# Optimization experiments

Hardware: AMD Instinct MI355X
Metric: run time of the kernel (lower is better)

The kernel has to match this reference:

```python
import jax, jax.numpy as jnp
import numpy as np

B = 256; NROIS = 200; IN = 200; HID = 128; L = 4; H = 8; RATIO = 0.5
K = int(np.ceil(RATIO * NROIS))        # SAGPooling top-k per graph = 100
N = B * NROIS                          # total nodes = 51200
DEG = 32; EPG = NROIS * DEG; E_EDGES = B * EPG  # 1,638,400 edges
EMB = HID * L                          # MHA embed dim = 512
DH = EMB // H

def _xavier(k, shape):
    fan_in, fan_out = shape[-2], shape[-1]
    lim = float(np.sqrt(6.0 / (fan_in + fan_out)))
    return jax.random.uniform(k, shape, jnp.float32, -lim, lim)

def setup_inputs() -> dict:
    key = jax.random.key(0)
    ks = jax.random.split(key, 16)
    x = jax.random.normal(ks[0], (N, IN), jnp.float32)
    # block-diagonal edge list: edges stay within each graph's node range
    src = jax.random.randint(ks[1], (E_EDGES,), 0, NROIS, jnp.int32)
    dst = jax.random.randint(ks[2], (E_EDGES,), 0, NROIS, jnp.int32)
    off = jnp.repeat(jnp.arange(B, dtype=jnp.int32) * NROIS, EPG)
    edge_index = jnp.stack([src + off, dst + off])
    edge_attr = jax.random.normal(ks[3], (E_EDGES,), jnp.float32)  # unused by the math
    batch = jnp.repeat(jnp.arange(B, dtype=jnp.int32), NROIS)
    return dict(
        x=x, edge_index=edge_index, edge_attr=edge_attr, batch=batch,
        gcn_w0=_xavier(ks[4], (IN, HID)),
        gcn_w=_xavier(ks[5], (L - 1, HID, HID)),
        gcn_b=jnp.zeros((L, HID), jnp.float32),
        lin1_w0=_xavier(ks[6], (IN + HID, HID)),
        lin1_w=_xavier(ks[7], (L - 1, 2 * HID, HID)),
        lin1_b=jnp.zeros((L, HID), jnp.float32),
        lin2_w=_xavier(ks[8], (L, HID, HID)),
        lin2_b=jnp.zeros((L, HID), jnp.float32),
        sag_w1=_xavier(ks[9], (HID, 1)),
        sag_w2=_xavier(ks[10], (HID, 1)),
        sag_b=jnp.zeros((1,), jnp.float32),
        mha_in_w=_xavier(ks[11], (3 * EMB, EMB)),
        mha_in_b=jnp.zeros((3 * EMB,), jnp.float32),
        mha_out_w=_xavier(ks[12], (EMB, EMB)),
        mha_out_b=jnp.zeros((EMB,), jnp.float32),
        fin_w=_xavier(ks[13], (EMB, HID)),
        fin_b=jnp.zeros((HID,), jnp.float32),
    )

def _gcn_conv(x, src, dst, W, b):
    xw = x @ W
    deg = jax.ops.segment_sum(jnp.ones_like(dst, jnp.float32), dst, num_segments=N) + 1.0
    dinv = jax.lax.rsqrt(deg)
    norm = dinv[src] * dinv[dst]                     # [E]
    agg = jax.ops.segment_sum(xw[src] * norm[:, None], dst, num_segments=N)
    agg = agg + xw * (dinv * dinv)[:, None]          # self-loop term
    return agg + b

def _gcblock(x, src, dst, gw, gb, l1w, l1b, l2w, l2b):
    x1 = jnp.tanh(_gcn_conv(x, src, dst, gw, gb))
    h = jnp.tanh(jnp.concatenate([x, x1], axis=1) @ l1w + l1b)
    return jnp.tanh(h @ l2w + l2b)

def _sag_pool_pad(z, src, dst, w1, w2, b):
    # SAGPooling score via PyG GraphConv (aggr='add'): lin_rel(sum_j x_j) + lin_root(x_i)
    neigh = jax.ops.segment_sum(z[src], dst, num_segments=N)
    score = (neigh @ w1)[:, 0] + b[0] + (z @ w2)[:, 0]        # [N]
    s3 = score.reshape(B, NROIS)
    vals, idx = jax.lax.top_k(s3, K)                           # [B,K]
    z3 = z.reshape(B, NROIS, HID)
    pooled = jnp.take_along_axis(z3, idx[:, :, None], axis=1) * jnp.tanh(vals)[:, :, None]
    zpad = jnp.zeros_like(z3).at[jnp.arange(B)[:, None], idx].set(pooled)
    return zpad.reshape(N, HID)

def reference(x, edge_index, edge_attr, batch,
              gcn_w0, gcn_w, gcn_b, lin1_w0, lin1_w, lin1_b, lin2_w, lin2_b,
              sag_w1, sag_w2, sag_b,
              mha_in_w, mha_in_b, mha_out_w, mha_out_b, fin_w, fin_b):
    src, dst = edge_index[0], edge_index[1]
    z = x
    pads = []
    for i in range(L):
        gw = gcn_w0 if i == 0 else gcn_w[i - 1]
        l1w = lin1_w0 if i == 0 else lin1_w[i - 1]
        z = _gcblock(z, src, dst, gw, gcn_b[i], l1w, lin1_b[i], lin2_w[i], lin2_b[i])
        pads.append(_sag_pool_pad(z, src, dst, sag_w1, sag_w2, sag_b))
    xc = jnp.concatenate(pads, axis=1).reshape(B, NROIS, EMB)   # [B,S,E]
    # MultiheadAttention (batch_first, eval mode -> no dropout)
    qkv = xc @ mha_in_w.T + mha_in_b                             # [B,S,3E]
    q, k, v = jnp.split(qkv, 3, axis=-1)
    def heads(t):
        return t.reshape(B, NROIS, H, DH).transpose(0, 2, 1, 3)  # [B,H,S,dh]
    q, k, v = heads(q), heads(k), heads(v)
    scores = jnp.einsum('bhqd,bhkd->bhqk', q, k) / np.sqrt(DH)
    attn = jax.nn.softmax(scores, axis=-1)                       # [B,H,S,S]
    o = jnp.einsum('bhqk,bhkd->bhqd', attn, v).transpose(0, 2, 1, 3).reshape(B, NROIS, EMB)
    o = o @ mha_out_w.T + mha_out_b
    attn_weights = attn.mean(axis=1)                             # avg over heads [B,S,S]
    # readout: global_mean_pool over each graph's nrois nodes
    pooled = o.mean(axis=1)                                      # [B,E]
    out = jnp.tanh(pooled @ fin_w + fin_b)                       # [B,HID]
    return out, attn_weights
```

## Files before the change

kernel.cpp:

```cpp
#include <hip/hip_runtime.h>
#include <hip/hip_fp16.h>


#define GB   256
#define SS   200
#define KIN  200
#define HD   128
#define NLAY 4
#define NHD  8
#define TOPK 100
#define NT   (GB * SS)
#define EPG_ 6400
#define NE_  (GB * EPG_)
#define EMB_ 512

typedef _Float16 half8 __attribute__((ext_vector_type(8)));
typedef _Float16 half4v __attribute__((ext_vector_type(4)));
typedef float floatx4 __attribute__((ext_vector_type(4)));

__global__ __launch_bounds__(256) void k_build_A(const int* __restrict__ src,
                                                 const int* __restrict__ dst,
                                                 float* __restrict__ A) {
  int e = blockIdx.x * 256 + threadIdx.x;
  if (e >= NE_) return;
  int d = dst[e], s = src[e];
  int b = d / SS;
  int dl = d - b * SS;
  int sl = s - b * SS;
  atomicAdd(&A[((size_t)b * SS + dl) * SS + sl], 1.0f);
}

__global__ __launch_bounds__(256) void k_dinv(const float* __restrict__ A,
                                              float* __restrict__ dinv) {
  int node = blockIdx.x * 4 + (threadIdx.x >> 6);
  int lane = threadIdx.x & 63;
  const float* r = A + (size_t)node * SS;
  float v = r[lane] + r[lane + 64] + r[lane + 128];
  if (lane < 8) v += r[lane + 192];
#pragma unroll
  for (int o = 32; o; o >>= 1) v += __shfl_xor(v, o);
  if (lane == 0) dinv[node] = rsqrtf(v + 1.0f);
}

__global__ __launch_bounds__(256) void k_prep_all(
    const float* __restrict__ gcn_w0, const float* __restrict__ gcn_w,
    const float* __restrict__ lin1_w0, const float* __restrict__ lin1_w,
    const float* __restrict__ lin2_w,
    __half* __restrict__ whi, __half* __restrict__ wlo) {
  const int mat = blockIdx.x >> 7;
  const int n   = blockIdx.x & 127;
  const int l = mat / 3, which = mat % 3;
  const float* src;
  int K, Kpad;
  if (which == 0) {
    K = l ? HD : KIN;  Kpad = l ? 128 : 256;
    src = l ? gcn_w + (size_t)(l - 1) * HD * HD : gcn_w0;
  } else if (which == 1) {
    K = l ? 2 * HD : KIN + HD;  Kpad = l ? 256 : 384;
    src = l ? lin1_w + (size_t)(l - 1) * 2 * HD * HD : lin1_w0;
  } else {
    K = HD;  Kpad = HD;
    src = lin2_w + (size_t)l * HD * HD;
  }
  int off = (l == 0) ? (which == 0 ? 0 : (which == 1 ? 32768 : 81920))
                     : 98304 + (l - 1) * 65536 +
                       (which == 0 ? 0 : (which == 1 ? 16384 : 49152));
  _Float16* wh = (_Float16*)whi + (size_t)off + (size_t)n * Kpad;
  _Float16* wl = (_Float16*)wlo + (size_t)off + (size_t)n * Kpad;
  for (int k = threadIdx.x; k < Kpad; k += 256) {
    float v = (k < K) ? src[(size_t)k * HD + n] : 0.f;
    _Float16 h = (_Float16)v;
    wh[k] = h;
    wl[k] = (_Float16)(v - (float)h);
  }
}

__global__ __launch_bounds__(256) void k_node_mfma(
    const float* __restrict__ in1, int k1,
    const float* __restrict__ in2,
    const __half* __restrict__ Whi, const __half* __restrict__ Wlo,
    int Kpad,
    const float* __restrict__ bias,
    float* __restrict__ out, int doTanh) {
  const int m0 = blockIdx.x * 64;
  const int t = threadIdx.x;
  const int wave = t >> 6, lane = t & 63;
  const int col = lane & 15, quad = lane >> 4;
  const int wm = (wave & 1) * 32;
  const int wn = (wave >> 1) * 64;
  __shared__ __align__(16) _Float16 Ah[64][72];
  __shared__ __align__(16) _Float16 Al[64][72];
  floatx4 acc[2][4] = {};
  const int lr = t >> 2;
  const int lk = (t & 3) * 16;
  const _Float16* Wh = (const _Float16*)Whi;
  const _Float16* Wl = (const _Float16*)Wlo;

  for (int k0 = 0; k0 < Kpad; k0 += 64) {
    __syncthreads();
#pragma unroll
    for (int q = 0; q < 4; ++q) {
      int kg = k0 + lk + q * 4;
      float4 v = {0.f, 0.f, 0.f, 0.f};
      if (kg < k1)
        v = *reinterpret_cast<const float4*>(&in1[(size_t)(m0 + lr) * k1 + kg]);
      else if (in2 && kg < k1 + HD)
        v = *reinterpret_cast<const float4*>(&in2[(size_t)(m0 + lr) * HD + (kg - k1)]);
      half4v h = {(_Float16)v.x, (_Float16)v.y, (_Float16)v.z, (_Float16)v.w};
      half4v lo = {(_Float16)(v.x - (float)h.x), (_Float16)(v.y - (float)h.y),
                   (_Float16)(v.z - (float)h.z), (_Float16)(v.w - (float)h.w)};
      *reinterpret_cast<half4v*>(&Ah[lr][lk + q * 4]) = h;
      *reinterpret_cast<half4v*>(&Al[lr][lk + q * 4]) = lo;
    }
    __syncthreads();
#pragma unroll
    for (int ks = 0; ks < 2; ++ks) {
      half8 ah[2], al[2], bh[4], bl[4];
#pragma unroll
      for (int i = 0; i < 2; ++i) {
        ah[i] = *reinterpret_cast<const half8*>(&Ah[wm + i * 16 + col][ks * 32 + quad * 8]);
        al[i] = *reinterpret_cast<const half8*>(&Al[wm + i * 16 + col][ks * 32 + quad * 8]);
      }
#pragma unroll
      for (int j = 0; j < 4; ++j) {
        const size_t wo = (size_t)(wn + j * 16 + col) * Kpad + k0 + ks * 32 + quad * 8;
        bh[j] = *reinterpret_cast<const half8*>(Wh + wo);
        bl[j] = *reinterpret_cast<const half8*>(Wl + wo);
      }
#pragma unroll
      for (int i = 0; i < 2; ++i)
#pragma unroll
        for (int j = 0; j < 4; ++j) {
          acc[i][j] = __builtin_amdgcn_mfma_f32_16x16x32_f16(ah[i], bh[j], acc[i][j], 0, 0, 0);
          acc[i][j] = __builtin_amdgcn_mfma_f32_16x16x32_f16(ah[i], bl[j], acc[i][j], 0, 0, 0);
          acc[i][j] = __builtin_amdgcn_mfma_f32_16x16x32_f16(al[i], bh[j], acc[i][j], 0, 0, 0);
        }
    }
  }
#pragma unroll
  for (int j = 0; j < 4; ++j) {
    int n = wn + j * 16 + col;
    float bb = bias ? bias[n] : 0.f;
#pragma unroll
    for (int i = 0; i < 2; ++i) {
      int rbase = m0 + wm + i * 16 + quad * 4;
#pragma unroll
      for (int r = 0; r < 4; ++r) {
        float v = acc[i][j][r] + bb;
        if (doTanh) v = tanhf(v);
        out[(size_t)(rbase + r) * HD + n] = v;
      }
    }
  }
}

__global__ __launch_bounds__(256) void k_agg_mfma(
    const float* __restrict__ A, const float* __restrict__ dinv,
    const float* __restrict__ xw, const float* __restrict__ bias,
    float* __restrict__ out) {
  const int b    = blockIdx.x >> 1;
  const int row0 = (blockIdx.x & 1) * 128;
  const int t = threadIdx.x;
  const int wave = t >> 6, lane = t & 63;
  const int col = lane & 15, quad = lane >> 4;
  const int wm = (wave & 1) * 64, wn = (wave >> 1) * 64;
  __shared__ __align__(16) _Float16 Ah[128][72];
  __shared__ __align__(16) _Float16 Al[128][72];
  __shared__ __align__(16) _Float16 Bh[128][72];
  __shared__ __align__(16) _Float16 Bl[128][72];
  __shared__ float dvs[256];
  dvs[t] = (t < SS) ? dinv[b * SS + t] : 0.f;
  floatx4 acc[4][4] = {};
  const float* Ab  = A  + (size_t)b * SS * SS;
  const float* xwb = xw + (size_t)b * SS * HD;
  const int lr = t >> 1, lk = (t & 1) * 32;
  const int d = row0 + lr;
  __syncthreads();
  const float dvd = (d < SS) ? dvs[d] : 0.f;

  for (int k0 = 0; k0 < 256; k0 += 64) {
    __syncthreads();
#pragma unroll
    for (int q = 0; q < 8; ++q) {
      int s = k0 + lk + q * 4;
      float4 v = {0.f, 0.f, 0.f, 0.f};
      if (d < SS && s < SS)
        v = *reinterpret_cast<const float4*>(&Ab[(size_t)d * SS + s]);
      float e0 = (v.x + ((s + 0 == d) ? 1.f : 0.f)) * dvd * dvs[(s + 0) & 255];
      float e1 = (v.y + ((s + 1 == d) ? 1.f : 0.f)) * dvd * dvs[(s + 1) & 255];
      float e2 = (v.z + ((s + 2 == d) ? 1.f : 0.f)) * dvd * dvs[(s + 2) & 255];
      float e3 = (v.w + ((s + 3 == d) ? 1.f : 0.f)) * dvd * dvs[(s + 3) & 255];
      half4v h = {(_Float16)e0, (_Float16)e1, (_Float16)e2, (_Float16)e3};
      half4v lo = {(_Float16)(e0 - (float)h.x), (_Float16)(e1 - (float)h.y),
                   (_Float16)(e2 - (float)h.z), (_Float16)(e3 - (float)h.w)};
      *reinterpret_cast<half4v*>(&Ah[lr][lk + q * 4]) = h;
      *reinterpret_cast<half4v*>(&Al[lr][lk + q * 4]) = lo;
    }
#pragma unroll
    for (int p = 0; p < 8; ++p) {
      int idx = t + p * 256;
      int c4 = idx & 31, ss = idx >> 5;
      int s = k0 + ss;
      float4 v = {0.f, 0.f, 0.f, 0.f};
      if (s < SS)
        v = *reinterpret_cast<const float4*>(&xwb[(size_t)s * HD + c4 * 4]);
      int ssx = ss ^ ((c4 & 7) << 3);
      float e[4] = {v.x, v.y, v.z, v.w};
#pragma unroll
      for (int j = 0; j < 4; ++j) {
        _Float16 h = (_Float16)e[j];
        Bh[c4 * 4 + j][ssx] = h;
        Bl[c4 * 4 + j][ssx] = (_Float16)(e[j] - (float)h);
      }
    }
    __syncthreads();
#pragma unroll
    for (int ks = 0; ks < 2; ++ks) {
      half8 ah[4], al[4], bh[4], bl[4];
#pragma unroll
      for (int i = 0; i < 4; ++i) {
        ah[i] = *reinterpret_cast<const half8*>(&Ah[wm + i * 16 + col][ks * 32 + quad * 8]);
        al[i] = *reinterpret_cast<const half8*>(&Al[wm + i * 16 + col][ks * 32 + quad * 8]);
      }
#pragma unroll
      for (int j = 0; j < 4; ++j) {
        int n = wn + j * 16 + col;
        int koff = (ks * 32 + quad * 8) ^ (((n >> 2) & 7) << 3);
        bh[j] = *reinterpret_cast<const half8*>(&Bh[n][koff]);
        bl[j] = *reinterpret_cast<const half8*>(&Bl[n][koff]);
      }
#pragma unroll
      for (int i = 0; i < 4; ++i)
#pragma unroll
        for (int j = 0; j < 4; ++j) {
          acc[i][j] = __builtin_amdgcn_mfma_f32_16x16x32_f16(ah[i], bh[j], acc[i][j], 0, 0, 0);
          acc[i][j] = __builtin_amdgcn_mfma_f32_16x16x32_f16(ah[i], bl[j], acc[i][j], 0, 0, 0);
          acc[i][j] = __builtin_amdgcn_mfma_f32_16x16x32_f16(al[i], bh[j], acc[i][j], 0, 0, 0);
        }
    }
  }
#pragma unroll
  for (int j = 0; j < 4; ++j) {
    int n = wn + j * 16 + col;
    float bb = bias[n];
#pragma unroll
    for (int i = 0; i < 4; ++i) {
      int rbase = row0 + wm + i * 16 + quad * 4;
#pragma unroll
      for (int r = 0; r < 4; ++r) {
        int row = rbase + r;
        if (row < SS)
          out[((size_t)b * SS + row) * HD + n] = tanhf(acc[i][j][r] + bb);
      }
    }
  }
}

__global__ __launch_bounds__(256) void k_sag(
    const float* __restrict__ z, const float* __restrict__ A,
    const float* __restrict__ w1, const float* __restrict__ w2,
    const float* __restrict__ sb, float* __restrict__ xc, int layer) {
  const int b = blockIdx.x, t = threadIdx.x;
  __shared__ float w1s[HD], w2s[HD];
  __shared__ float zw1[SS], sc[SS], fac[SS];
  if (t < HD) { w1s[t] = w1[t]; w2s[t] = w2[t]; }
  __syncthreads();
  float a2 = 0.f;
  if (t < SS) {
    const float4* zr = reinterpret_cast<const float4*>(&z[((size_t)b * SS + t) * HD]);
    float a1 = 0.f;
#pragma unroll
    for (int q = 0; q < HD / 4; ++q) {
      float4 v = zr[q];
      a1 += v.x * w1s[4 * q] + v.y * w1s[4 * q + 1] + v.z * w1s[4 * q + 2] + v.w * w1s[4 * q + 3];
      a2 += v.x * w2s[4 * q] + v.y * w2s[4 * q + 1] + v.z * w2s[4 * q + 2] + v.w * w2s[4 * q + 3];
    }
    zw1[t] = a1;
  }
  __syncthreads();
  if (t < SS) {
    float s = sb[0] + a2;
    const float4* ar = reinterpret_cast<const float4*>(&A[((size_t)b * SS + t) * SS]);
#pragma unroll 5
    for (int q = 0; q < SS / 4; ++q) {
      float4 v = ar[q];
      s += v.x * zw1[4 * q] + v.y * zw1[4 * q + 1] + v.z * zw1[4 * q + 2] + v.w * zw1[4 * q + 3];
    }
    sc[t] = s;
  }
  __syncthreads();
  if (t < SS) {
    float si = sc[t];
    int cnt = 0;
    for (int j = 0; j < SS; ++j) {
      float sj = sc[j];
      cnt += (sj > si || (sj == si && j < t)) ? 1 : 0;
    }
    fac[t] = (cnt < TOPK) ? tanhf(si) : 0.f;
  }
  __syncthreads();
  for (int idx = t; idx < SS * HD; idx += 256) {
    int row = idx >> 7, c = idx & 127;
    xc[((size_t)b * SS + row) * EMB_ + layer * HD + c] =
        fac[row] * z[((size_t)b * SS + row) * HD + c];
  }
}

__global__ __launch_bounds__(256) void k_proj(
    const float* __restrict__ xc, const float* __restrict__ Win,
    const float* __restrict__ bin, __half* __restrict__ QKh) {
  const int wg = (blockIdx.x & 7) * 400 + (blockIdx.x >> 3);
  const int bm = wg >> 3;
  const int bn = wg & 7;
  const int m0 = bm * 128, n0 = bn * 128;
  const int t    = threadIdx.x;
  const int wave = t >> 6, lane = t & 63;
  const int col  = lane & 15, quad = lane >> 4;
  const int wm = (wave & 1) * 64;
  const int wn = (wave >> 1) * 64;
  __shared__ __align__(16) _Float16 As[128][72];
  __shared__ __align__(16) _Float16 Bs[128][72];
  floatx4 acc[4][4] = {};
  const int lr = t >> 1;
  const int lk = (t & 1) * 32;

  for (int k0 = 0; k0 < EMB_; k0 += 64) {
    __syncthreads();
    const float4* ga = reinterpret_cast<const float4*>(&xc [(size_t)(m0 + lr) * EMB_ + k0 + lk]);
    const float4* gb = reinterpret_cast<const float4*>(&Win[(size_t)(n0 + lr) * EMB_ + k0 + lk]);
#pragma unroll
    for (int q = 0; q < 8; ++q) {
      float4 va = ga[q];
      half4v ha = {(_Float16)va.x, (_Float16)va.y, (_Float16)va.z, (_Float16)va.w};
      *reinterpret_cast<half4v*>(&As[lr][lk + q * 4]) = ha;
      float4 vb = gb[q];
      half4v hb = {(_Float16)vb.x, (_Float16)vb.y, (_Float16)vb.z, (_Float16)vb.w};
      *reinterpret_cast<half4v*>(&Bs[lr][lk + q * 4]) = hb;
    }
    __syncthreads();
#pragma unroll
    for (int ks = 0; ks < 2; ++ks) {
      half8 af[4], bf[4];
#pragma unroll
      for (int i = 0; i < 4; ++i)
        af[i] = *reinterpret_cast<const half8*>(&As[wm + i * 16 + col][ks * 32 + quad * 8]);
#pragma unroll
      for (int j = 0; j < 4; ++j)
        bf[j] = *reinterpret_cast<const half8*>(&Bs[wn + j * 16 + col][ks * 32 + quad * 8]);
#pragma unroll
      for (int i = 0; i < 4; ++i)
#pragma unroll
        for (int j = 0; j < 4; ++j)
          acc[i][j] = __builtin_amdgcn_mfma_f32_16x16x32_f16(af[i], bf[j], acc[i][j], 0, 0, 0);
    }
  }
#pragma unroll
  for (int j = 0; j < 4; ++j) {
    int c = n0 + wn + j * 16 + col;
    float bb = bin[c];
#pragma unroll
    for (int i = 0; i < 4; ++i) {
      int rbase = m0 + wm + i * 16 + quad * 4;
#pragma unroll
      for (int r = 0; r < 4; ++r)
        QKh[(size_t)(rbase + r) * 1024 + c] = __float2half(acc[i][j][r] + bb);
    }
  }
}

__global__ __launch_bounds__(256) void k_attn(
    const __half* __restrict__ QKh,
    float* __restrict__ cpbuf,
    float* __restrict__ attn) {
  const int b  = blockIdx.x / 13;
  const int it = blockIdx.x % 13;
  const int i0 = it * 16;
  const int rows = (SS - i0 >= 16) ? 16 : (SS - i0);
  const int t    = threadIdx.x;
  const int wave = t >> 6;
  const int lane = t & 63;
  const int col  = lane & 15;
  const int quad = lane >> 4;

  __shared__ __align__(16) _Float16 kS[208][72];
  __shared__ __align__(16) _Float16 qS[16][72];
  __shared__ __align__(16) float    Ss[16][212];

  float am[13];
  int   soff[13];
  int   kmax = 0;
#pragma unroll
  for (int k = 0; k < 13; ++k) {
    int idx = t + (k << 8);
    am[k] = 0.f;
    if (idx < rows * 200) {
      int i = idx / 200;
      soff[k] = idx + 12 * i;
      kmax = k + 1;
    } else soff[k] = 0;
  }

  const size_t gbase = (size_t)b * SS * 1024;

  for (int h = 0; h < NHD; ++h) {
    __syncthreads();
#pragma unroll
    for (int p = 0; p < 7; ++p) {
      int li = t + (p << 8);
      if (li < 1664) {
        int j = li >> 3, c = li & 7;
        float4 v = {0.f, 0.f, 0.f, 0.f};
        if (j < SS) v = *reinterpret_cast<const float4*>(
            &QKh[gbase + (size_t)j * 1024 + 512 + h * 64 + c * 8]);
        *reinterpret_cast<float4*>(&kS[j][c * 8]) = v;
      }
    }
    if (t < 128) {
      int i = t >> 3, c = t & 7;
      int gi = i0 + i;
      float4 v = {0.f, 0.f, 0.f, 0.f};
      if (gi < SS) v = *reinterpret_cast<const float4*>(
          &QKh[gbase + (size_t)gi * 1024 + h * 64 + c * 8]);
      *reinterpret_cast<float4*>(&qS[i][c * 8]) = v;
    }
    __syncthreads();
    half8 a0 = *reinterpret_cast<const half8*>(&qS[col][quad * 8]);
    half8 a1 = *reinterpret_cast<const half8*>(&qS[col][32 + quad * 8]);
#pragma unroll
    for (int m = 0; m < 4; ++m) {
      int jt = wave + m * 4;
      if (jt < 13) {
        const int j0 = jt * 16;
        half8 b0 = *reinterpret_cast<const half8*>(&kS[j0 + col][quad * 8]);
        half8 b1 = *reinterpret_cast<const half8*>(&kS[j0 + col][32 + quad * 8]);
        floatx4 acc = {0.f, 0.f, 0.f, 0.f};
        acc = __builtin_amdgcn_mfma_f32_16x16x32_f16(a0, b0, acc, 0, 0, 0);
        acc = __builtin_amdgcn_mfma_f32_16x16x32_f16(a1, b1, acc, 0, 0, 0);
#pragma unroll
        for (int r = 0; r < 4; ++r)
          Ss[quad * 4 + r][j0 + col] = acc[r] * 0.125f;
      }
    }
    __syncthreads();
#pragma unroll
    for (int ri = 0; ri < 4; ++ri) {
      int r = wave * 4 + ri;
      if (r < rows) {
        float* srow = &Ss[r][0];
        float s0 = srow[lane], s1 = srow[lane + 64], s2 = srow[lane + 128];
        float s3 = (lane < 8) ? srow[lane + 192] : -1e30f;
        float mx = fmaxf(fmaxf(s0, s1), fmaxf(s2, s3));
#pragma unroll
        for (int o = 32; o; o >>= 1) mx = fmaxf(mx, __shfl_xor(mx, o));
        float e0 = __expf(s0 - mx), e1 = __expf(s1 - mx), e2 = __expf(s2 - mx);
        float e3 = (lane < 8) ? __expf(s3 - mx) : 0.f;
        float sum = e0 + e1 + e2 + e3;
#pragma unroll
        for (int o = 32; o; o >>= 1) sum += __shfl_xor(sum, o);
        float rl = 1.0f / sum;
        srow[lane] = e0 * rl; srow[lane + 64] = e1 * rl; srow[lane + 128] = e2 * rl;
        if (lane < 8) srow[lane + 192] = e3 * rl;
      }
    }
    __syncthreads();
    const float* sflat = &Ss[0][0];
#pragma unroll
    for (int k = 0; k < 13; ++k)
      if (k < kmax) am[k] += sflat[soff[k]] * 0.125f;
    if (t < SS) {
      float s = 0.f;
      for (int i = 0; i < rows; ++i) s += Ss[i][t];
      atomicAdd(&cpbuf[((size_t)b * NHD + h) * SS + t], s);
    }
  }
  float* abase = &attn[((size_t)b * SS + i0) * SS];
#pragma unroll
  for (int k = 0; k < 13; ++k)
    if (k < kmax) abase[t + (k << 8)] = am[k];
}

__global__ __launch_bounds__(256) void k_pool(
    const float* __restrict__ xc, const float* __restrict__ cpbuf,
    const float* __restrict__ Win, const float* __restrict__ bin,
    float* __restrict__ pooled) {
  const int b = blockIdx.x, t = threadIdx.x;
  __shared__ float cps[NHD][SS];
  __shared__ float tvs[NHD][EMB_];
  for (int idx = t; idx < NHD * SS; idx += 256) {
    int h = idx / SS, j = idx - h * SS;
    cps[h][j] = cpbuf[((size_t)b * NHD + h) * SS + j];
  }
  __syncthreads();
  const float* xcb = xc + (size_t)b * SS * EMB_;
  float a0[NHD] = {0.f}, a1[NHD] = {0.f};
  for (int j = 0; j < SS; ++j) {
    float x0 = xcb[(size_t)j * EMB_ + t];
    float x1 = xcb[(size_t)j * EMB_ + t + 256];
#pragma unroll
    for (int h = 0; h < NHD; ++h) {
      float c = cps[h][j];
      a0[h] += c * x0; a1[h] += c * x1;
    }
  }
#pragma unroll
  for (int h = 0; h < NHD; ++h) { tvs[h][t] = a0[h]; tvs[h][t + 256] = a1[h]; }
  __syncthreads();
  const int wv = t >> 6, lane = t & 63;
  for (int e = wv; e < EMB_; e += 4) {
    int h = e >> 6;
    const float* wr = Win + (size_t)(2 * EMB_ + e) * EMB_;
    float s = 0.f;
#pragma unroll
    for (int q = 0; q < 8; ++q) s += wr[lane + q * 64] * tvs[h][lane + q * 64];
#pragma unroll
    for (int o = 32; o; o >>= 1) s += __shfl_xor(s, o);
    if (lane == 0) pooled[(size_t)b * EMB_ + e] = bin[2 * EMB_ + e] * (float)SS + s;
  }
}

__global__ __launch_bounds__(256) void k_final(
    const float* __restrict__ pooled, const float* __restrict__ Wout,
    const float* __restrict__ bout, const float* __restrict__ finw,
    const float* __restrict__ finb, float* __restrict__ out) {
  const int b = blockIdx.x, t = threadIdx.x;
  __shared__ float pl[EMB_], po[EMB_];
  for (int k = t; k < EMB_; k += 256) pl[k] = pooled[(size_t)b * EMB_ + k] * (1.0f / (float)SS);
  __syncthreads();
  for (int e = t; e < EMB_; e += 256) {
    const float* wr = &Wout[(size_t)e * EMB_];
    float a = bout[e];
    for (int k = 0; k < EMB_; ++k) a += wr[k] * pl[k];
    po[e] = a;
  }
  __syncthreads();
  if (t < HD) {
    float a = finb[t];
    for (int e = 0; e < EMB_; ++e) a += po[e] * finw[(size_t)e * HD + t];
    out[(size_t)b * HD + t] = tanhf(a);
  }
}

extern "C" void kernel_launch(void* const* d_in, const int* in_sizes, int n_in,
                              void* d_out, int out_size, void* d_ws, size_t ws_size,
                              hipStream_t stream) {
  const float* x         = (const float*)d_in[0];
  const int*   ei        = (const int*)d_in[1];
  const float* gcn_w0    = (const float*)d_in[4];
  const float* gcn_w     = (const float*)d_in[5];
  const float* gcn_b     = (const float*)d_in[6];
  const float* lin1_w0   = (const float*)d_in[7];
  const float* lin1_w    = (const float*)d_in[8];
  const float* lin1_b    = (const float*)d_in[9];
  const float* lin2_w    = (const float*)d_in[10];
  const float* lin2_b    = (const float*)d_in[11];
  const float* sag_w1    = (const float*)d_in[12];
  const float* sag_w2    = (const float*)d_in[13];
  const float* sag_b     = (const float*)d_in[14];
  const float* mha_in_w  = (const float*)d_in[15];
  const float* mha_in_b  = (const float*)d_in[16];
  const float* mha_out_w = (const float*)d_in[17];
  const float* mha_out_b = (const float*)d_in[18];
  const float* fin_w     = (const float*)d_in[19];
  const float* fin_b     = (const float*)d_in[20];

  float* ws     = (float*)d_ws;
  float* dinv   = ws;
  float* Araw   = dinv + NT;
  float* buf0   = Araw + (size_t)GB * SS * SS;
  float* buf1   = buf0 + (size_t)NT * HD;
  float* zbuf   = buf1 + (size_t)NT * HD;
  float* xcbuf  = zbuf + (size_t)NT * HD;
  float* pooled = xcbuf + (size_t)NT * EMB_;
  __half* QKh  = (__half*)Araw;
  float* cpbuf = Araw + 26214400;

  float* outp = (float*)d_out;
  float* attn = outp + (size_t)GB * HD;

  __half* whi = (__half*)attn;
  __half* wlo = whi + 294912;

  hipMemsetAsync(Araw, 0, (size_t)GB * SS * SS * sizeof(float), stream);

  k_prep_all<<<12 * 128, 256, 0, stream>>>(gcn_w0, gcn_w, lin1_w0, lin1_w, lin2_w, whi, wlo);
  k_build_A<<<NE_ / 256, 256, 0, stream>>>(ei, ei + NE_, Araw);
  k_dinv<<<NT / 4, 256, 0, stream>>>(Araw, dinv);

  static const int KPg[4]  = {256, 128, 128, 128};
  static const int KP1[4]  = {384, 256, 256, 256};
  static const int OFFg[4] = {0, 98304, 163840, 229376};
  static const int OFF1[4] = {32768, 114688, 180224, 245760};
  static const int OFF2[4] = {81920, 147456, 212992, 278528};

  for (int l = 0; l < NLAY; ++l) {
    const float* zin = (l == 0) ? x : zbuf;
    int k1 = (l == 0) ? KIN : HD;
    k_node_mfma<<<NT / 64, 256, 0, stream>>>(zin, k1, nullptr,
                                             whi + OFFg[l], wlo + OFFg[l], KPg[l],
                                             nullptr, buf0, 0);
    k_agg_mfma<<<GB * 2, 256, 0, stream>>>(Araw, dinv, buf0, gcn_b + l * HD, buf1);
    k_node_mfma<<<NT / 64, 256, 0, stream>>>(zin, k1, buf1,
                                             whi + OFF1[l], wlo + OFF1[l], KP1[l],
                                             lin1_b + l * HD, buf0, 1);
    k_node_mfma<<<NT / 64, 256, 0, stream>>>(buf0, HD, nullptr,
                                             whi + OFF2[l], wlo + OFF2[l], HD,
                                             lin2_b + l * HD, zbuf, 1);
    k_sag<<<GB, 256, 0, stream>>>(zbuf, Araw, sag_w1, sag_w2, sag_b, xcbuf, l);
  }

  hipMemsetAsync(cpbuf, 0, (size_t)GB * NHD * SS * sizeof(float), stream);
  k_proj<<<(NT / 128) * 8, 256, 0, stream>>>(xcbuf, mha_in_w, mha_in_b, QKh);
  k_attn<<<GB * 13, 256, 0, stream>>>(QKh, cpbuf, attn);
  k_pool<<<GB, 256, 0, stream>>>(xcbuf, cpbuf, mha_in_w, mha_in_b, pooled);
  k_final<<<GB, 256, 0, stream>>>(pooled, mha_out_w, mha_out_b, fin_w, fin_b, outp);
}
```

Baseline: 1.624 ms.

## Store xc as fp16 hi/lo pairs and read QK/MHA operands directly from global

k_sag now writes the concatenated pooled features as fp16 high/low pairs instead of fp32. A new prep kernel converts the MHA input weights to fp16 once. k_proj then feeds its MFMA fragments straight from global memory with no LDS staging or in-loop conversion, and k_attn likewise reads Q/K fragments from global, with its block order swizzled for cache locality. k_pool rebuilds fp32 values from the hi/lo pair. The aim is to cut conversion work, shared-memory traffic and barriers, at the cost of uncoalesced-looking global fragment loads that rely on L2 hits.

```diff
diff --git a/kernel.cpp b/kernel.cpp
--- a/kernel.cpp
+++ b/kernel.cpp
@@ -73,6 +73,14 @@
     wh[k] = h;
     wl[k] = (_Float16)(v - (float)h);
   }
+}
+
+__global__ __launch_bounds__(256) void k_prep_w16(const float* __restrict__ W,
+                                                  __half* __restrict__ W16) {
+  int i = blockIdx.x * 256 + threadIdx.x;
+  float4 v = reinterpret_cast<const float4*>(W)[i];
+  half4v h = {(_Float16)v.x, (_Float16)v.y, (_Float16)v.z, (_Float16)v.w};
+  *reinterpret_cast<half4v*>((_Float16*)W16 + (size_t)i * 4) = h;
 }
 
 __global__ __launch_bounds__(256) void k_node_mfma(
@@ -259,7 +267,8 @@
 __global__ __launch_bounds__(256) void k_sag(
     const float* __restrict__ z, const float* __restrict__ A,
     const float* __restrict__ w1, const float* __restrict__ w2,
-    const float* __restrict__ sb, float* __restrict__ xc, int layer) {
+    const float* __restrict__ sb,
+    __half* __restrict__ xch, __half* __restrict__ xcl, int layer) {
   const int b = blockIdx.x, t = threadIdx.x;
   __shared__ float w1s[HD], w2s[HD];
   __shared__ float zw1[SS], sc[SS], fac[SS];
@@ -299,60 +308,54 @@
     fac[t] = (cnt < TOPK) ? tanhf(si) : 0.f;
   }
   __syncthreads();
+  _Float16* xh = (_Float16*)xch;
+  _Float16* xl = (_Float16*)xcl;
   for (int idx = t; idx < SS * HD; idx += 256) {
     int row = idx >> 7, c = idx & 127;
-    xc[((size_t)b * SS + row) * EMB_ + layer * HD + c] =
-        fac[row] * z[((size_t)b * SS + row) * HD + c];
+    float v = fac[row] * z[((size_t)b * SS + row) * HD + c];
+    _Float16 h = (_Float16)v;
+    size_t o = ((size_t)b * SS + row) * EMB_ + layer * HD + c;
+    xh[o] = h;
+    xl[o] = (_Float16)(v - (float)h);
   }
 }
 
 __global__ __launch_bounds__(256) void k_proj(
-    const float* __restrict__ xc, const float* __restrict__ Win,
+    const __half* __restrict__ xch, const __half* __restrict__ Win16,
     const float* __restrict__ bin, __half* __restrict__ QKh) {
   const int wg = (blockIdx.x & 7) * 400 + (blockIdx.x >> 3);
   const int bm = wg >> 3;
   const int bn = wg & 7;
   const int m0 = bm * 128, n0 = bn * 128;
-  const int t    = threadIdx.x;
+  const int t = threadIdx.x;
   const int wave = t >> 6, lane = t & 63;
-  const int col  = lane & 15, quad = lane >> 4;
+  const int col = lane & 15, quad = lane >> 4;
   const int wm = (wave & 1) * 64;
   const int wn = (wave >> 1) * 64;
-  __shared__ __align__(16) _Float16 As[128][72];
-  __shared__ __align__(16) _Float16 Bs[128][72];
   floatx4 acc[4][4] = {};
-  const int lr = t >> 1;
-  const int lk = (t & 1) * 32;
-
-  for (int k0 = 0; k0 < EMB_; k0 += 64) {
-    __syncthreads();
-    const float4* ga = reinterpret_cast<const float4*>(&xc [(size_t)(m0 + lr) * EMB_ + k0 + lk]);
-    const float4* gb = reinterpret_cast<const float4*>(&Win[(size_t)(n0 + lr) * EMB_ + k0 + lk]);
-#pragma unroll
-    for (int q = 0; q < 8; ++q) {
-      float4 va = ga[q];
-      half4v ha = {(_Float16)va.x, (_Float16)va.y, (_Float16)va.z, (_Float16)va.w};
-      *reinterpret_cast<half4v*>(&As[lr][lk + q * 4]) = ha;
-      float4 vb = gb[q];
-      half4v hb = {(_Float16)vb.x, (_Float16)vb.y, (_Float16)vb.z, (_Float16)vb.w};
-      *reinterpret_cast<half4v*>(&Bs[lr][lk + q * 4]) = hb;
-    }
-    __syncthreads();
-#pragma unroll
-    for (int ks = 0; ks < 2; ++ks) {
-      half8 af[4], bf[4];
-#pragma unroll
-      for (int i = 0; i < 4; ++i)
-        af[i] = *reinterpret_cast<const half8*>(&As[wm + i * 16 + col][ks * 32 + quad * 8]);
+  const _Float16* X = (const _Float16*)xch;
+  const _Float16* W = (const _Float16*)Win16;
+  const _Float16* xa[4];
+  const _Float16* wb[4];
+#pragma unroll
+  for (int i = 0; i < 4; ++i)
+    xa[i] = X + (size_t)(m0 + wm + i * 16 + col) * EMB_ + quad * 8;
+#pragma unroll
+  for (int j = 0; j < 4; ++j)
+    wb[j] = W + (size_t)(n0 + wn + j * 16 + col) * EMB_ + quad * 8;
+
+#pragma unroll 4
+  for (int k0 = 0; k0 < EMB_; k0 += 32) {
+    half8 af[4], bf[4];
+#pragma unroll
+    for (int i = 0; i < 4; ++i) af[i] = *reinterpret_cast<const half8*>(xa[i] + k0);
+#pragma unroll
+    for (int j = 0; j < 4; ++j) bf[j] = *reinterpret_cast<const half8*>(wb[j] + k0);
+#pragma unroll
+    for (int i = 0; i < 4; ++i)
 #pragma unroll
       for (int j = 0; j < 4; ++j)
-        bf[j] = *reinterpret_cast<const half8*>(&Bs[wn + j * 16 + col][ks * 32 + quad * 8]);
-#pragma unroll
-      for (int i = 0; i < 4; ++i)
-#pragma unroll
-        for (int j = 0; j < 4; ++j)
-          acc[i][j] = __builtin_amdgcn_mfma_f32_16x16x32_f16(af[i], bf[j], acc[i][j], 0, 0, 0);
-    }
+        acc[i][j] = __builtin_amdgcn_mfma_f32_16x16x32_f16(af[i], bf[j], acc[i][j], 0, 0, 0);
   }
 #pragma unroll
   for (int j = 0; j < 4; ++j) {
@@ -372,8 +375,9 @@
     const __half* __restrict__ QKh,
     float* __restrict__ cpbuf,
     float* __restrict__ attn) {
-  const int b  = blockIdx.x / 13;
-  const int it = blockIdx.x % 13;
+  const int bx = (blockIdx.x & 7) * 416 + (blockIdx.x >> 3);
+  const int b  = bx / 13;
+  const int it = bx % 13;
   const int i0 = it * 16;
   const int rows = (SS - i0 >= 16) ? 16 : (SS - i0);
   const int t    = threadIdx.x;
@@ -382,9 +386,7 @@
   const int col  = lane & 15;
   const int quad = lane >> 4;
 
-  __shared__ __align__(16) _Float16 kS[208][72];
-  __shared__ __align__(16) _Float16 qS[16][72];
-  __shared__ __align__(16) float    Ss[16][212];
+  __shared__ __align__(16) float Ss[16][212];
 
   float am[13];
   int   soff[13];
@@ -400,45 +402,31 @@
     } else soff[k] = 0;
   }
 
-  const size_t gbase = (size_t)b * SS * 1024;
+  const _Float16* Qbase = (const _Float16*)QKh + (size_t)b * SS * 1024;
+  const _Float16* qrow = Qbase + (size_t)(i0 + col) * 1024 + quad * 8;
+  const _Float16* krow[4];
+#pragma unroll
+  for (int m = 0; m < 4; ++m) {
+    int jt = wave + m * 4;
+    krow[m] = Qbase + (size_t)(jt * 16 + col) * 1024 + 512 + quad * 8;
+  }
 
   for (int h = 0; h < NHD; ++h) {
-    __syncthreads();
-#pragma unroll
-    for (int p = 0; p < 7; ++p) {
-      int li = t + (p << 8);
-      if (li < 1664) {
-        int j = li >> 3, c = li & 7;
-        float4 v = {0.f, 0.f, 0.f, 0.f};
-        if (j < SS) v = *reinterpret_cast<const float4*>(
-            &QKh[gbase + (size_t)j * 1024 + 512 + h * 64 + c * 8]);
-        *reinterpret_cast<float4*>(&kS[j][c * 8]) = v;
-      }
-    }
-    if (t < 128) {
-      int i = t >> 3, c = t & 7;
-      int gi = i0 + i;
-      float4 v = {0.f, 0.f, 0.f, 0.f};
-      if (gi < SS) v = *reinterpret_cast<const float4*>(
-          &QKh[gbase + (size_t)gi * 1024 + h * 64 + c * 8]);
-      *reinterpret_cast<float4*>(&qS[i][c * 8]) = v;
-    }
-    __syncthreads();
-    half8 a0 = *reinterpret_cast<const half8*>(&qS[col][quad * 8]);
-    half8 a1 = *reinterpret_cast<const half8*>(&qS[col][32 + quad * 8]);
+    const int hoff = h * 64;
+    half8 a0 = *reinterpret_cast<const half8*>(qrow + hoff);
+    half8 a1 = *reinterpret_cast<const half8*>(qrow + hoff + 32);
 #pragma unroll
     for (int m = 0; m < 4; ++m) {
       int jt = wave + m * 4;
       if (jt < 13) {
-        const int j0 = jt * 16;
-        half8 b0 = *reinterpret_cast<const half8*>(&kS[j0 + col][quad * 8]);
-        half8 b1 = *reinterpret_cast<const half8*>(&kS[j0 + col][32 + quad * 8]);
+        half8 b0 = *reinterpret_cast<const half8*>(krow[m] + hoff);
+        half8 b1 = *reinterpret_cast<const half8*>(krow[m] + hoff + 32);
         floatx4 acc = {0.f, 0.f, 0.f, 0.f};
         acc = __builtin_amdgcn_mfma_f32_16x16x32_f16(a0, b0, acc, 0, 0, 0);
         acc = __builtin_amdgcn_mfma_f32_16x16x32_f16(a1, b1, acc, 0, 0, 0);
 #pragma unroll
         for (int r = 0; r < 4; ++r)
-          Ss[quad * 4 + r][j0 + col] = acc[r] * 0.125f;
+          Ss[quad * 4 + r][jt * 16 + col] = acc[r] * 0.125f;
       }
     }
     __syncthreads();
@@ -472,6 +460,7 @@
       for (int i = 0; i < rows; ++i) s += Ss[i][t];
       atomicAdd(&cpbuf[((size_t)b * NHD + h) * SS + t], s);
     }
+    __syncthreads();
   }
   float* abase = &attn[((size_t)b * SS + i0) * SS];
 #pragma unroll
@@ -480,7 +469,8 @@
 }
 
 __global__ __launch_bounds__(256) void k_pool(
-    const float* __restrict__ xc, const float* __restrict__ cpbuf,
+    const __half* __restrict__ xch, const __half* __restrict__ xcl,
+    const float* __restrict__ cpbuf,
     const float* __restrict__ Win, const float* __restrict__ bin,
     float* __restrict__ pooled) {
   const int b = blockIdx.x, t = threadIdx.x;
@@ -491,11 +481,12 @@
     cps[h][j] = cpbuf[((size_t)b * NHD + h) * SS + j];
   }
   __syncthreads();
-  const float* xcb = xc + (size_t)b * SS * EMB_;
+  const _Float16* xh = (const _Float16*)xch + (size_t)b * SS * EMB_;
+  const _Float16* xl = (const _Float16*)xcl + (size_t)b * SS * EMB_;
   float a0[NHD] = {0.f}, a1[NHD] = {0.f};
   for (int j = 0; j < SS; ++j) {
-    float x0 = xcb[(size_t)j * EMB_ + t];
-    float x1 = xcb[(size_t)j * EMB_ + t + 256];
+    float x0 = (float)xh[(size_t)j * EMB_ + t] + (float)xl[(size_t)j * EMB_ + t];
+    float x1 = (float)xh[(size_t)j * EMB_ + t + 256] + (float)xl[(size_t)j * EMB_ + t + 256];
 #pragma unroll
     for (int h = 0; h < NHD; ++h) {
       float c = cps[h][j];
@@ -569,20 +560,24 @@
   float* buf0   = Araw + (size_t)GB * SS * SS;
   float* buf1   = buf0 + (size_t)NT * HD;
   float* zbuf   = buf1 + (size_t)NT * HD;
-  float* xcbuf  = zbuf + (size_t)NT * HD;
-  float* pooled = xcbuf + (size_t)NT * EMB_;
+  float* xcf    = zbuf + (size_t)NT * HD;
+  __half* xch   = (__half*)xcf;
+  __half* xcl   = xch + (size_t)NT * EMB_;
+  float* pooled = xcf + (size_t)NT * EMB_;
   __half* QKh  = (__half*)Araw;
   float* cpbuf = Araw + 26214400;
 
   float* outp = (float*)d_out;
   float* attn = outp + (size_t)GB * HD;
 
-  __half* whi = (__half*)attn;
-  __half* wlo = whi + 294912;
+  __half* whi   = (__half*)attn;
+  __half* wlo   = whi + 294912;
+  __half* Win16 = wlo + 294912;
 
   hipMemsetAsync(Araw, 0, (size_t)GB * SS * SS * sizeof(float), stream);
 
   k_prep_all<<<12 * 128, 256, 0, stream>>>(gcn_w0, gcn_w, lin1_w0, lin1_w, lin2_w, whi, wlo);
+  k_prep_w16<<<512, 256, 0, stream>>>(mha_in_w, Win16);
   k_build_A<<<NE_ / 256, 256, 0, stream>>>(ei, ei + NE_, Araw);
   k_dinv<<<NT / 4, 256, 0, stream>>>(Araw, dinv);
 
@@ -605,12 +600,12 @@
     k_node_mfma<<<NT / 64, 256, 0, stream>>>(buf0, HD, nullptr,
                                              whi + OFF2[l], wlo + OFF2[l], HD,
                                              lin2_b + l * HD, zbuf, 1);
-    k_sag<<<GB, 256, 0, stream>>>(zbuf, Araw, sag_w1, sag_w2, sag_b, xcbuf, l);
+    k_sag<<<GB, 256, 0, stream>>>(zbuf, Araw, sag_w1, sag_w2, sag_b, xch, xcl, l);
   }
 
   hipMemsetAsync(cpbuf, 0, (size_t)GB * NHD * SS * sizeof(float), stream);
-  k_proj<<<(NT / 128) * 8, 256, 0, stream>>>(xcbuf, mha_in_w, mha_in_b, QKh);
+  k_proj<<<(NT / 128) * 8, 256, 0, stream>>>(xch, Win16, mha_in_b, QKh);
   k_attn<<<GB * 13, 256, 0, stream>>>(QKh, cpbuf, attn);
-  k_pool<<<GB, 256, 0, stream>>>(xcbuf, cpbuf, mha_in_w, mha_in_b, pooled);
+  k_pool<<<GB, 256, 0, stream>>>(xch, xcl, cpbuf, mha_in_w, mha_in_b, pooled);
   k_final<<<GB, 256, 0, stream>>>(pooled, mha_out_w, mha_out_b, fin_w, fin_b, outp);
 }
```

After: 1.575 ms. 1.03x faster.
